# Kernel optimization log

Measured on AMD Instinct MI355X. Metric: run time of the kernel, lower is better.

The kernel has to match this reference:

```python
import jax, jax.numpy as jnp
import numpy as np

EMB = 128
HID = 256
VOCAB = 32000
B, LS, LT = 16, 256, 128


def _lstm(x_seq, h0, c0, Wk, Wr, b):
    """Keras-style LSTM (gate order i,f,g,o). x_seq: [B,T,D] -> ([B,T,H], h, c)."""
    xz = jnp.einsum('btd,dg->btg', x_seq, Wk) + b  # precompute input projection

    def step(carry, zt):
        h, c = carry
        z = zt + h @ Wr  # [B,4H]
        i, f, g, o = jnp.split(z, 4, axis=-1)
        c = jax.nn.sigmoid(f) * c + jax.nn.sigmoid(i) * jnp.tanh(g)
        h = jax.nn.sigmoid(o) * jnp.tanh(c)
        return (h, c), h

    (h, c), hs = jax.lax.scan(step, (h0, c0), xz.transpose(1, 0, 2))
    return hs.transpose(1, 0, 2), h, c


def setup_inputs() -> dict:
    key = jax.random.key(0)
    ks = jax.random.split(key, 12)
    sd_e = 1.0 / np.sqrt(EMB)
    sd_h = 1.0 / np.sqrt(HID)
    return {
        'x': jax.random.randint(ks[0], (B, LS), 0, VOCAB, dtype=jnp.int32),
        'y': jax.random.randint(ks[1], (B, LT), 0, VOCAB, dtype=jnp.int32),
        'enc_emb': jax.random.normal(ks[2], (VOCAB, EMB), jnp.float32) * 0.05,
        'enc_Wk': jax.random.normal(ks[3], (EMB, 4 * HID), jnp.float32) * sd_e,
        'enc_Wr': jax.random.normal(ks[4], (HID, 4 * HID), jnp.float32) * sd_h,
        'enc_b': jnp.zeros((4 * HID,), jnp.float32),
        'dec_emb': jax.random.normal(ks[5], (VOCAB, EMB), jnp.float32) * 0.05,
        'dec_Wk': jax.random.normal(ks[6], (EMB, 4 * HID), jnp.float32) * sd_e,
        'dec_Wr': jax.random.normal(ks[7], (HID, 4 * HID), jnp.float32) * sd_h,
        'dec_b': jnp.zeros((4 * HID,), jnp.float32),
        'Wout': jax.random.normal(ks[8], (2 * HID, VOCAB), jnp.float32) * (1.0 / np.sqrt(2 * HID)),
        'bout': jnp.zeros((VOCAB,), jnp.float32),
    }


def reference(x, y, enc_emb, enc_Wk, enc_Wr, enc_b, dec_emb, dec_Wk, dec_Wr, dec_b, Wout, bout):
    # ---- Encoder ----
    xe = enc_emb[x]  # [B,LS,EMB]
    z0 = jnp.zeros((x.shape[0], HID), jnp.float32)
    H, h, c = _lstm(xe, z0, z0, enc_Wk, enc_Wr, enc_b)  # H: [B,LS,HID]
    # ---- Decoder (teacher forcing) ----
    ye = dec_emb[y]  # [B,LT,EMB]
    S, hT, cT = _lstm(ye, h, c, dec_Wk, dec_Wr, dec_b)  # [B,LT,HID]
    S_ = jnp.concatenate([h[:, None, :], S[:, :-1, :]], axis=1)  # shifted states
    # Keras Attention (dot, no scale): A = softmax(S_ H^T) H
    scores = jnp.einsum('btd,bsd->bts', S_, H)  # [B,LT,LS]
    A = jnp.einsum('bts,bsd->btd', jax.nn.softmax(scores, axis=-1), H)
    feat = jnp.concatenate([S, A], axis=-1)  # [B,LT,2*HID]
    probs = jax.nn.softmax(feat @ Wout + bout, axis=-1)  # [B,LT,VOCAB]
    return probs
```

## Files before the change

### kernel.cpp

```cpp
#include <hip/hip_runtime.h>
#include <hip/hip_bf16.h>
#include <math.h>

#define BB    16
#define LS    256
#define LT    128
#define EMB   128
#define HID   256
#define G4    1024
#define VOCAB 32000

#define NSL   8
#define XROWS 112

typedef __attribute__((ext_vector_type(8))) short bf16x8;
typedef __attribute__((ext_vector_type(4))) float f32x4;
typedef __attribute__((ext_vector_type(4))) int   i32x4;
typedef unsigned short ushort_t;
typedef unsigned int uint_t;

__device__ inline float sigf(float x)      { return 1.0f / (1.0f + __expf(-x)); }
__device__ inline float tanhfast(float x)  { return 1.0f - 2.0f / (1.0f + __expf(2.0f * x)); }
__device__ inline ushort_t bf16_rne(float f) {
  __hip_bfloat16 h = __float2bfloat16(f);
  return *(ushort_t*)&h;
}

__global__ __launch_bounds__(256) void embed_proj_kernel(
    const int* __restrict__ x, const int* __restrict__ y,
    const float* __restrict__ eemb, const float* __restrict__ eWk,
    const float* __restrict__ eb,
    const float* __restrict__ demb, const float* __restrict__ dWk,
    const float* __restrict__ db,
    float* __restrict__ xze, float* __restrict__ xzd)
{
  const bool enc = blockIdx.x < 128;
  const int* idx = enc ? x : y;
  const float* emb = enc ? eemb : demb;
  const float* Wk  = enc ? eWk  : dWk;
  const float* bias= enc ? eb   : db;
  float* xz        = enc ? xze  : xzd;
  const int row0 = (enc ? blockIdx.x : blockIdx.x - 128) * 32;

  __shared__ float e[32][EMB];
  const int tid = threadIdx.x;

  for (int i = tid; i < 32 * EMB; i += 256) {
    int r = i >> 7, k = i & 127;
    int token = idx[row0 + r];
    e[r][k] = emb[(size_t)token * EMB + k];
  }
  __syncthreads();

  float acc[4][32];
#pragma unroll
  for (int q = 0; q < 4; ++q)
#pragma unroll
    for (int r = 0; r < 32; ++r) acc[q][r] = 0.0f;

  for (int k = 0; k < EMB; ++k) {
    float w0 = Wk[(size_t)k * G4 + 0 * 256 + tid];
    float w1 = Wk[(size_t)k * G4 + 1 * 256 + tid];
    float w2 = Wk[(size_t)k * G4 + 2 * 256 + tid];
    float w3 = Wk[(size_t)k * G4 + 3 * 256 + tid];
#pragma unroll
    for (int r = 0; r < 32; ++r) {
      float ev = e[r][k];
      acc[0][r] = fmaf(ev, w0, acc[0][r]);
      acc[1][r] = fmaf(ev, w1, acc[1][r]);
      acc[2][r] = fmaf(ev, w2, acc[2][r]);
      acc[3][r] = fmaf(ev, w3, acc[3][r]);
    }
  }
#pragma unroll
  for (int q = 0; q < 4; ++q) {
    float bb = bias[q * 256 + tid];
#pragma unroll
    for (int r = 0; r < 32; ++r)
      xz[(size_t)(row0 + r) * G4 + q * 256 + tid] = acc[q][r] + bb;
  }
}

__global__ __launch_bounds__(512, 1) void lstm_kernel(
    const float* __restrict__ xz,
    const float* __restrict__ Wr,
    const float* __restrict__ h0,
    int h0_stride,
    const float* __restrict__ cinit,
    float* __restrict__ Hout,
    float* __restrict__ c_fin,
    i32x4* __restrict__ fmb,
    int kid,
    int T)
{
  const int b    = blockIdx.x & (BB - 1);
  const int s    = blockIdx.x >> 4;
  const int tid  = threadIdx.x;
  const int lane = tid & 63;
  const int quarter = tid >> 7;
  const int col  = tid & 127;
  const int gate = col >> 5, u = col & 31;

  __shared__ float part[2][4][128];
  __shared__ float xbuf[XROWS][128];

  float w_r[64];
  {
    const float* wp = Wr + (size_t)(quarter * 64) * G4 + gate * 256 + s * 32 + u;
#pragma unroll
    for (int j = 0; j < 64; ++j) w_r[j] = wp[(size_t)j * G4];
  }

  const int i0 = quarter * 64 + lane;
  float hv = 0.0f;
  if (h0) hv = h0[(size_t)b * h0_stride + i0];

  float cs0 = 0.0f, cs1 = 0.0f;
  if (tid < 16 && cinit) {
    cs0 = cinit[b * HID + s * 32 + 2 * tid];
    cs1 = cinit[b * HID + s * 32 + 2 * tid + 1];
  }

  const int c0i = i0 >> 1;
  const int sel = i0 & 1;

  int tp = XROWS;
  for (int t = 0; t < T; ++t, ++tp) {
    if (tp >= XROWS) {
      __syncthreads();
      tp = 0;
      for (int tt = quarter; tt < XROWS; tt += 4) {
        int ts = t + tt;
        if (ts < T)
          xbuf[tt][col] = xz[((size_t)b * T + ts) * G4 + gate * 256 + s * 32 + u];
      }
    }

    float a0 = 0.0f, a1 = 0.0f, a2 = 0.0f, a3 = 0.0f;
#pragma unroll
    for (int j = 0; j < 64; j += 4) {
      a0 = fmaf(__int_as_float(__builtin_amdgcn_readlane(__float_as_int(hv), j + 0)), w_r[j + 0], a0);
      a1 = fmaf(__int_as_float(__builtin_amdgcn_readlane(__float_as_int(hv), j + 1)), w_r[j + 1], a1);
      a2 = fmaf(__int_as_float(__builtin_amdgcn_readlane(__float_as_int(hv), j + 2)), w_r[j + 2], a2);
      a3 = fmaf(__int_as_float(__builtin_amdgcn_readlane(__float_as_int(hv), j + 3)), w_r[j + 3], a3);
    }
    part[t & 1][quarter][col] = (a0 + a1) + (a2 + a3);
    __syncthreads();

    const int stamp = (t + 1) | (kid << 20);
    const size_t slot = (size_t)(b * 2 + (t & 1)) * 128;

    if (tid < 16) {
      const int ua = 2 * tid, ub = ua + 1;
      const float (*pp)[128] = part[t & 1];
      float p0a = pp[0][ua] + pp[1][ua] + pp[2][ua] + pp[3][ua];
      float p0b = pp[0][ub] + pp[1][ub] + pp[2][ub] + pp[3][ub];
      float p1a = pp[0][32 + ua] + pp[1][32 + ua] + pp[2][32 + ua] + pp[3][32 + ua];
      float p1b = pp[0][32 + ub] + pp[1][32 + ub] + pp[2][32 + ub] + pp[3][32 + ub];
      float p2a = pp[0][64 + ua] + pp[1][64 + ua] + pp[2][64 + ua] + pp[3][64 + ua];
      float p2b = pp[0][64 + ub] + pp[1][64 + ub] + pp[2][64 + ub] + pp[3][64 + ub];
      float p3a = pp[0][96 + ua] + pp[1][96 + ua] + pp[2][96 + ua] + pp[3][96 + ua];
      float p3b = pp[0][96 + ub] + pp[1][96 + ub] + pp[2][96 + ub] + pp[3][96 + ub];
      float2 xg0 = *(const float2*)&xbuf[tp][ua];
      float2 xg1 = *(const float2*)&xbuf[tp][32 + ua];
      float2 xg2 = *(const float2*)&xbuf[tp][64 + ua];
      float2 xg3 = *(const float2*)&xbuf[tp][96 + ua];

      float zi0 = p0a + xg0.x, zi1 = p0b + xg0.y;
      float zf0 = p1a + xg1.x, zf1 = p1b + xg1.y;
      float zg0 = p2a + xg2.x, zg1 = p2b + xg2.y;
      float zo0 = p3a + xg3.x, zo1 = p3b + xg3.y;

      cs0 = fmaf(sigf(zf0), cs0, sigf(zi0) * tanhfast(zg0));
      cs1 = fmaf(sigf(zf1), cs1, sigf(zi1) * tanhfast(zg1));
      float ha = sigf(zo0) * tanhfast(cs0);
      float hb = sigf(zo1) * tanhfast(cs1);

      *(float2*)&Hout[((size_t)b * T + t) * HID + s * 32 + ua] = make_float2(ha, hb);

      i32x4 ch;
      ch.x = __float_as_int(ha);
      ch.y = __float_as_int(hb);
      ch.z = ch.x ^ ch.y ^ stamp;
      ch.w = 0;
      const i32x4* fd = fmb + slot + s * 16 + tid;
      asm volatile("global_store_dwordx4 %0, %1, off sc0 sc1"
                   :: "v"(fd), "v"(ch) : "memory");
    }
    __syncthreads();

    if (t + 1 < T) {
      const i32x4* fp = fmb + slot + c0i;
      i32x4 v;
      for (;;) {
        asm volatile("global_load_dwordx4 %0, %1, off sc0 sc1\n\t"
                     "s_waitcnt vmcnt(0)"
                     : "=&v"(v) : "v"(fp) : "memory");
        if (v.z == (v.x ^ v.y ^ stamp)) break;
      }
      hv = __int_as_float(sel ? v.y : v.x);
    }
  }
  if (c_fin && tid < 16)
    *(float2*)&c_fin[b * HID + s * 32 + 2 * tid] = make_float2(cs0, cs1);
}

__global__ __launch_bounds__(256) void mid_kernel(
    const float* __restrict__ W, ushort_t* __restrict__ WT,
    const float* __restrict__ Henc, const float* __restrict__ S,
    __hip_bfloat16* __restrict__ featB)
{
  const int tid = threadIdx.x;

  if (blockIdx.x < 4000) {
    __shared__ float tile[64][65];
    const int nt = blockIdx.x % 500;
    const int kt = blockIdx.x / 500;
    const int n0 = nt * 64, k0 = kt * 64;
    const int r = tid >> 6, c = tid & 63;

#pragma unroll
    for (int q = 0; q < 16; ++q) {
      int kk = q * 4 + r;
      tile[kk][c] = W[(size_t)(k0 + kk) * VOCAB + n0 + c];
    }
    __syncthreads();

    const int nl = tid >> 2;
    const int seg = (tid & 3) * 16;
    uint_t o[8];
#pragma unroll
    for (int j = 0; j < 8; ++j) {
      uint_t lo = bf16_rne(tile[seg + 2 * j][nl]);
      uint_t hi = bf16_rne(tile[seg + 2 * j + 1][nl]);
      o[j] = lo | (hi << 16);
    }
    ushort_t* dst = WT + (size_t)(n0 + nl) * 512 + k0 + seg;
    ((uint4*)dst)[0] = make_uint4(o[0], o[1], o[2], o[3]);
    ((uint4*)dst)[1] = make_uint4(o[4], o[5], o[6], o[7]);
  } else {
    __shared__ float srow[HID];
    __shared__ float p[LS];
    __shared__ float sm[LS];

    const int m = blockIdx.x - 4000;
    const int b = m >> 7, t = m & (LT - 1);

    const float* s_ = (t == 0) ? (Henc + ((size_t)b * LS + (LS - 1)) * HID)
                               : (S + (size_t)(m - 1) * HID);
    srow[tid] = s_[tid];
    __syncthreads();

    const float4* h4 = (const float4*)(Henc + ((size_t)b * LS + tid) * HID);
    const float4* s4 = (const float4*)srow;
    float sc = 0.0f;
#pragma unroll 8
    for (int k = 0; k < HID / 4; ++k) {
      float4 a = h4[k], q = s4[k];
      sc += a.x * q.x + a.y * q.y + a.z * q.z + a.w * q.w;
    }
    sm[tid] = sc;
    __syncthreads();
    for (int st = 128; st > 0; st >>= 1) {
      if (tid < st) sm[tid] = fmaxf(sm[tid], sm[tid + st]);
      __syncthreads();
    }
    float mx = sm[0];
    __syncthreads();
    float e = __expf(sc - mx);
    p[tid] = e;
    sm[tid] = e;
    __syncthreads();
    for (int st = 128; st > 0; st >>= 1) {
      if (tid < st) sm[tid] += sm[tid + st];
      __syncthreads();
    }
    float inv = 1.0f / sm[0];

    float a_d = 0.0f;
#pragma unroll 4
    for (int s2 = 0; s2 < LS; ++s2)
      a_d = fmaf(p[s2], Henc[((size_t)b * LS + s2) * HID + tid], a_d);
    a_d *= inv;

    featB[(size_t)m * (2 * HID) + tid]       = __float2bfloat16(S[(size_t)m * HID + tid]);
    featB[(size_t)m * (2 * HID) + HID + tid] = __float2bfloat16(a_d);
  }
}

__global__ __launch_bounds__(256) void proj_exp_kernel(
    const ushort_t* __restrict__ A, const ushort_t* __restrict__ BT,
    const float* __restrict__ bout, float* __restrict__ rowsum,
    float* __restrict__ out)
{
  __shared__ ushort_t Ab[2][128 * 64];
  __shared__ ushort_t Bb[2][128 * 64];

  const int bid = blockIdx.x;
  const int k2 = (bid & 7) * 500 + (bid >> 3);
  const int mt = k2 & 15, nt = k2 >> 4;
  const int m0 = mt * 128, n0 = nt * 128;
  const int tid = threadIdx.x;
  const int wave = tid >> 6, lane = tid & 63;
  const int wm = wave >> 1, wn = wave & 1;
  const int r = lane & 15, kg = lane >> 4;

  const ushort_t* Ag = A + (size_t)m0 * 512;
  const ushort_t* Bg = BT + (size_t)n0 * 512;

  f32x4 acc[4][4];
#pragma unroll
  for (int i = 0; i < 4; ++i)
#pragma unroll
    for (int j = 0; j < 4; ++j) acc[i][j] = (f32x4){0.f, 0.f, 0.f, 0.f};

#define STAGE(kc, buf)                                                       \
  {                                                                          \
    _Pragma("unroll")                                                        \
    for (int q = 0; q < 4; ++q) {                                            \
      int L = q * 256 + tid;                                                 \
      int row_ = L >> 3, seg_ = L & 7;                                       \
      int so_ = row_ * 64 + ((seg_ ^ (row_ & 7)) << 3);                      \
      uint4 va_ = *(const uint4*)(Ag + (size_t)row_ * 512 + (kc) * 64 + seg_ * 8); \
      uint4 vb_ = *(const uint4*)(Bg + (size_t)row_ * 512 + (kc) * 64 + seg_ * 8); \
      *(uint4*)&Ab[buf][so_] = va_;                                          \
      *(uint4*)&Bb[buf][so_] = vb_;                                          \
    }                                                                        \
  }

  STAGE(0, 0);
  __syncthreads();

  for (int kc = 0; kc < 8; ++kc) {
    const int cur = kc & 1;
    if (kc < 7) STAGE(kc + 1, cur ^ 1);
#pragma unroll
    for (int ks = 0; ks < 2; ++ks) {
      bf16x8 a[4], b[4];
      const int seg = ks * 4 + kg;
#pragma unroll
      for (int i = 0; i < 4; ++i) {
        int row = wm * 64 + i * 16 + r;
        a[i] = *(const bf16x8*)&Ab[cur][row * 64 + ((seg ^ (row & 7)) << 3)];
      }
#pragma unroll
      for (int j = 0; j < 4; ++j) {
        int row = wn * 64 + j * 16 + r;
        b[j] = *(const bf16x8*)&Bb[cur][row * 64 + ((seg ^ (row & 7)) << 3)];
      }
#pragma unroll
      for (int i = 0; i < 4; ++i)
#pragma unroll
        for (int j = 0; j < 4; ++j)
          acc[i][j] = __builtin_amdgcn_mfma_f32_16x16x32_bf16(a[i], b[j], acc[i][j], 0, 0, 0);
    }
    __syncthreads();
  }
#undef STAGE

  float bv[4];
#pragma unroll
  for (int j = 0; j < 4; ++j) bv[j] = bout[n0 + wn * 64 + j * 16 + r];

#pragma unroll
  for (int i = 0; i < 4; ++i)
#pragma unroll
    for (int q = 0; q < 4; ++q) {
      const int row = m0 + wm * 64 + i * 16 + kg * 4 + q;
      float v = 0.0f;
#pragma unroll
      for (int j = 0; j < 4; ++j) {
        float e = __expf(acc[i][j][q] + bv[j]);
        out[(size_t)row * VOCAB + n0 + wn * 64 + j * 16 + r] = e;
        v += e;
      }
#pragma unroll
      for (int msk = 1; msk < 16; msk <<= 1) v += __shfl_xor(v, msk, 64);
      if (r == 0) atomicAdd(&rowsum[row], v);
    }
}

__global__ __launch_bounds__(256) void scale_kernel(
    float* __restrict__ out, const float* __restrict__ rowsum)
{
  const int row = blockIdx.x >> 2;
  const int seg = blockIdx.x & 3;
  const float s = 1.0f / rowsum[row];
  float4* o4 = (float4*)(out + (size_t)row * VOCAB) + seg * 2000;
  for (int i = threadIdx.x; i < 2000; i += 256) {
    float4 v = o4[i];
    v.x *= s; v.y *= s; v.z *= s; v.w *= s;
    o4[i] = v;
  }
}

extern "C" void kernel_launch(void* const* d_in, const int* in_sizes, int n_in,
                              void* d_out, int out_size, void* d_ws, size_t ws_size,
                              hipStream_t stream) {
  (void)in_sizes; (void)n_in; (void)out_size; (void)ws_size;

  const int*   x       = (const int*)d_in[0];
  const int*   y       = (const int*)d_in[1];
  const float* enc_emb = (const float*)d_in[2];
  const float* enc_Wk  = (const float*)d_in[3];
  const float* enc_Wr  = (const float*)d_in[4];
  const float* enc_b   = (const float*)d_in[5];
  const float* dec_emb = (const float*)d_in[6];
  const float* dec_Wk  = (const float*)d_in[7];
  const float* dec_Wr  = (const float*)d_in[8];
  const float* dec_b   = (const float*)d_in[9];
  const float* Wout    = (const float*)d_in[10];
  const float* bout    = (const float*)d_in[11];
  float* out = (float*)d_out;
  char*  ws  = (char*)d_ws;

  size_t off = 0;
  float* xz_enc = (float*)(ws + off); off += (size_t)BB * LS * G4 * 4;
  float* xz_dec = (float*)(ws + off); off += (size_t)BB * LT * G4 * 4;
  float* Henc   = (float*)(ws + off); off += (size_t)BB * LS * HID * 4;
  float* S      = (float*)(ws + off); off += (size_t)BB * LT * HID * 4;
  __hip_bfloat16* featB = (__hip_bfloat16*)(ws + off);
  off += (size_t)BB * LT * 2 * HID * 2;
  ushort_t* WoutT = (ushort_t*)(ws + off); off += (size_t)VOCAB * 512 * 2;
  float* c_fin  = (float*)(ws + off); off += (size_t)BB * HID * 4;
  size_t zero_base = off;
  float* rowsum = (float*)(ws + off); off += (size_t)BB * LT * 4;
  i32x4* fmb    = (i32x4*)(ws + off); off += (size_t)BB * 2 * 128 * 16;
  size_t zero_len = off - zero_base;

  hipMemsetAsync(ws + zero_base, 0, zero_len, stream);

  embed_proj_kernel<<<192, 256, 0, stream>>>(
      x, y, enc_emb, enc_Wk, enc_b, dec_emb, dec_Wk, dec_b, xz_enc, xz_dec);

  lstm_kernel<<<NSL * BB, 512, 0, stream>>>(
      xz_enc, enc_Wr, nullptr, 0, nullptr, Henc, c_fin, fmb, 0, LS);

  lstm_kernel<<<NSL * BB, 512, 0, stream>>>(
      xz_dec, dec_Wr, Henc + (size_t)(LS - 1) * HID, LS * HID, c_fin,
      S, nullptr, fmb, 1, LT);

  mid_kernel<<<4000 + BB * LT, 256, 0, stream>>>(
      Wout, WoutT, Henc, S, (__hip_bfloat16*)featB);

  proj_exp_kernel<<<16 * 250, 256, 0, stream>>>(
      (const ushort_t*)featB, WoutT, bout, rowsum, out);
  scale_kernel<<<4 * BB * LT, 256, 0, stream>>>(out, rowsum);
}
```

Measured before the change: 1.099 ms.

## Overlap encoder LSTM with Wout prepack and decoder embedding in one launch

Splits the embedding projection so the encoder input projection runs first. A combined launch then runs the latency-bound encoder LSTM blocks alongside the Wout transpose/bf16 prepack and the decoder input projection, so those independent jobs fill otherwise idle CUs. The attention part of the old mid kernel becomes its own kernel. The LSTM flag poll now keeps two loads in flight to cut spin latency. The risk is that the 128 LSTM blocks, which talk to each other through the flag mailbox, may not all be resident at once if filler blocks take the CUs first, which could slow progress or deadlock. The extra blocks also compete for memory bandwidth.

```diff
diff --git a/kernel.cpp b/kernel.cpp
--- a/kernel.cpp
+++ b/kernel.cpp
@@ -12,6 +12,7 @@
 
 #define NSL   8
 #define XROWS 112
+#define LSTM_POOL (4096 + XROWS * 128 * 4)
 
 typedef __attribute__((ext_vector_type(8))) short bf16x8;
 typedef __attribute__((ext_vector_type(4))) float f32x4;
@@ -26,24 +27,13 @@
   return *(ushort_t*)&h;
 }
 
-__global__ __launch_bounds__(256) void embed_proj_kernel(
-    const int* __restrict__ x, const int* __restrict__ y,
-    const float* __restrict__ eemb, const float* __restrict__ eWk,
-    const float* __restrict__ eb,
-    const float* __restrict__ demb, const float* __restrict__ dWk,
-    const float* __restrict__ db,
-    float* __restrict__ xze, float* __restrict__ xzd)
-{
-  const bool enc = blockIdx.x < 128;
-  const int* idx = enc ? x : y;
-  const float* emb = enc ? eemb : demb;
-  const float* Wk  = enc ? eWk  : dWk;
-  const float* bias= enc ? eb   : db;
-  float* xz        = enc ? xze  : xzd;
-  const int row0 = (enc ? blockIdx.x : blockIdx.x - 128) * 32;
-
-  __shared__ float e[32][EMB];
-  const int tid = threadIdx.x;
+__device__ __forceinline__ void embed_body(
+    char* pool, int row0, int tid,
+    const int* __restrict__ idx, const float* __restrict__ emb,
+    const float* __restrict__ Wk, const float* __restrict__ bias,
+    float* __restrict__ xz)
+{
+  float (*e)[EMB] = (float (*)[EMB])pool;
 
   for (int i = tid; i < 32 * EMB; i += 256) {
     int r = i >> 7, k = i & 127;
@@ -81,28 +71,55 @@
   }
 }
 
-__global__ __launch_bounds__(512, 1) void lstm_kernel(
-    const float* __restrict__ xz,
-    const float* __restrict__ Wr,
-    const float* __restrict__ h0,
-    int h0_stride,
+__device__ __forceinline__ void prepack_body(
+    char* pool, int tileIdx, int tid,
+    const float* __restrict__ W, ushort_t* __restrict__ WT)
+{
+  float (*tile)[65] = (float (*)[65])pool;
+  const int nt = tileIdx % 500;
+  const int kt = tileIdx / 500;
+  const int n0 = nt * 64, k0 = kt * 64;
+  const int r = tid >> 6, c = tid & 63;
+
+#pragma unroll
+  for (int q = 0; q < 16; ++q) {
+    int kk = q * 4 + r;
+    tile[kk][c] = W[(size_t)(k0 + kk) * VOCAB + n0 + c];
+  }
+  __syncthreads();
+
+  const int nl = tid >> 2;
+  const int seg = (tid & 3) * 16;
+  uint_t o[8];
+#pragma unroll
+  for (int j = 0; j < 8; ++j) {
+    uint_t lo = bf16_rne(tile[seg + 2 * j][nl]);
+    uint_t hi = bf16_rne(tile[seg + 2 * j + 1][nl]);
+    o[j] = lo | (hi << 16);
+  }
+  ushort_t* dst = WT + (size_t)(n0 + nl) * 512 + k0 + seg;
+  ((uint4*)dst)[0] = make_uint4(o[0], o[1], o[2], o[3]);
+  ((uint4*)dst)[1] = make_uint4(o[4], o[5], o[6], o[7]);
+}
+
+__device__ __forceinline__ void lstm_body(
+    char* pool, int bid,
+    const float* __restrict__ xz, const float* __restrict__ Wr,
+    const float* __restrict__ h0, int h0_stride,
     const float* __restrict__ cinit,
-    float* __restrict__ Hout,
-    float* __restrict__ c_fin,
-    i32x4* __restrict__ fmb,
-    int kid,
-    int T)
-{
-  const int b    = blockIdx.x & (BB - 1);
-  const int s    = blockIdx.x >> 4;
+    float* __restrict__ Hout, float* __restrict__ c_fin,
+    i32x4* __restrict__ fmb, int kid, int T)
+{
+  float (*part)[4][128] = (float (*)[4][128])pool;
+  float (*xbuf)[128]    = (float (*)[128])(pool + 4096);
+
+  const int b    = bid & (BB - 1);
+  const int s    = bid >> 4;
   const int tid  = threadIdx.x;
   const int lane = tid & 63;
   const int quarter = tid >> 7;
   const int col  = tid & 127;
   const int gate = col >> 5, u = col & 31;
-
-  __shared__ float part[2][4][128];
-  __shared__ float xbuf[XROWS][128];
 
   float w_r[64];
   {
@@ -191,13 +208,22 @@
 
     if (t + 1 < T) {
       const i32x4* fp = fmb + slot + c0i;
-      i32x4 v;
+      i32x4 va, vb, v;
+      asm volatile("global_load_dwordx4 %0, %1, off sc0 sc1"
+                   : "=v"(va) : "v"(fp) : "memory");
+      asm volatile("global_load_dwordx4 %0, %1, off sc0 sc1"
+                   : "=v"(vb) : "v"(fp) : "memory");
       for (;;) {
-        asm volatile("global_load_dwordx4 %0, %1, off sc0 sc1\n\t"
-                     "s_waitcnt vmcnt(0)"
-                     : "=&v"(v) : "v"(fp) : "memory");
-        if (v.z == (v.x ^ v.y ^ stamp)) break;
+        asm volatile("s_waitcnt vmcnt(1)" : "+v"(va) :: "memory");
+        if (va.z == (va.x ^ va.y ^ stamp)) { v = va; break; }
+        asm volatile("global_load_dwordx4 %0, %1, off sc0 sc1"
+                     : "=v"(va) : "v"(fp) : "memory");
+        asm volatile("s_waitcnt vmcnt(1)" : "+v"(vb) :: "memory");
+        if (vb.z == (vb.x ^ vb.y ^ stamp)) { v = vb; break; }
+        asm volatile("global_load_dwordx4 %0, %1, off sc0 sc1"
+                     : "=v"(vb) : "v"(fp) : "memory");
       }
+      asm volatile("s_waitcnt vmcnt(0)" : "+v"(va), "+v"(vb) :: "memory");
       hv = __int_as_float(sel ? v.y : v.x);
     }
   }
@@ -205,87 +231,102 @@
     *(float2*)&c_fin[b * HID + s * 32 + 2 * tid] = make_float2(cs0, cs1);
 }
 
-__global__ __launch_bounds__(256) void mid_kernel(
-    const float* __restrict__ W, ushort_t* __restrict__ WT,
+__global__ __launch_bounds__(256) void embed_enc_kernel(
+    const int* __restrict__ x, const float* __restrict__ emb,
+    const float* __restrict__ Wk, const float* __restrict__ bias,
+    float* __restrict__ xz)
+{
+  __shared__ float poolf[32 * EMB];
+  embed_body((char*)poolf, blockIdx.x * 32, threadIdx.x, x, emb, Wk, bias, xz);
+}
+
+__global__ __launch_bounds__(512, 1) void enc_stage_kernel(
+    const float* __restrict__ xz_enc, const float* __restrict__ enc_Wr,
+    float* __restrict__ Henc, float* __restrict__ c_fin,
+    i32x4* __restrict__ fmb,
+    const float* __restrict__ Wout, ushort_t* __restrict__ WoutT,
+    const int* __restrict__ y, const float* __restrict__ dec_emb,
+    const float* __restrict__ dec_Wk, const float* __restrict__ dec_b,
+    float* __restrict__ xz_dec)
+{
+  extern __shared__ char pool[];
+  const int bid = blockIdx.x;
+  if (bid < 128) {
+    lstm_body(pool, bid, xz_enc, enc_Wr, nullptr, 0, nullptr,
+              Henc, c_fin, fmb, 0, LS);
+  } else if (bid < 2128) {
+    const int half = threadIdx.x >> 8, t256 = threadIdx.x & 255;
+    prepack_body(pool + half * 16640, 2 * (bid - 128) + half, t256, Wout, WoutT);
+  } else {
+    const int half = threadIdx.x >> 8, t256 = threadIdx.x & 255;
+    embed_body(pool + half * 16384, ((bid - 2128) * 2 + half) * 32, t256,
+               y, dec_emb, dec_Wk, dec_b, xz_dec);
+  }
+}
+
+__global__ __launch_bounds__(512, 1) void lstm_kernel(
+    const float* __restrict__ xz, const float* __restrict__ Wr,
+    const float* __restrict__ h0, int h0_stride,
+    const float* __restrict__ cinit,
+    float* __restrict__ Hout, float* __restrict__ c_fin,
+    i32x4* __restrict__ fmb, int kid, int T)
+{
+  extern __shared__ char pool[];
+  lstm_body(pool, blockIdx.x, xz, Wr, h0, h0_stride, cinit,
+            Hout, c_fin, fmb, kid, T);
+}
+
+__global__ __launch_bounds__(256) void attn_kernel(
     const float* __restrict__ Henc, const float* __restrict__ S,
     __hip_bfloat16* __restrict__ featB)
 {
+  const int m = blockIdx.x;
+  const int b = m >> 7, t = m & (LT - 1);
   const int tid = threadIdx.x;
 
-  if (blockIdx.x < 4000) {
-    __shared__ float tile[64][65];
-    const int nt = blockIdx.x % 500;
-    const int kt = blockIdx.x / 500;
-    const int n0 = nt * 64, k0 = kt * 64;
-    const int r = tid >> 6, c = tid & 63;
-
-#pragma unroll
-    for (int q = 0; q < 16; ++q) {
-      int kk = q * 4 + r;
-      tile[kk][c] = W[(size_t)(k0 + kk) * VOCAB + n0 + c];
-    }
+  __shared__ float srow[HID];
+  __shared__ float p[LS];
+  __shared__ float sm[LS];
+
+  const float* s_ = (t == 0) ? (Henc + ((size_t)b * LS + (LS - 1)) * HID)
+                             : (S + (size_t)(m - 1) * HID);
+  srow[tid] = s_[tid];
+  __syncthreads();
+
+  const float4* h4 = (const float4*)(Henc + ((size_t)b * LS + tid) * HID);
+  const float4* s4 = (const float4*)srow;
+  float sc = 0.0f;
+#pragma unroll 8
+  for (int k = 0; k < HID / 4; ++k) {
+    float4 a = h4[k], q = s4[k];
+    sc += a.x * q.x + a.y * q.y + a.z * q.z + a.w * q.w;
+  }
+  sm[tid] = sc;
+  __syncthreads();
+  for (int st = 128; st > 0; st >>= 1) {
+    if (tid < st) sm[tid] = fmaxf(sm[tid], sm[tid + st]);
     __syncthreads();
-
-    const int nl = tid >> 2;
-    const int seg = (tid & 3) * 16;
-    uint_t o[8];
-#pragma unroll
-    for (int j = 0; j < 8; ++j) {
-      uint_t lo = bf16_rne(tile[seg + 2 * j][nl]);
-      uint_t hi = bf16_rne(tile[seg + 2 * j + 1][nl]);
-      o[j] = lo | (hi << 16);
-    }
-    ushort_t* dst = WT + (size_t)(n0 + nl) * 512 + k0 + seg;
-    ((uint4*)dst)[0] = make_uint4(o[0], o[1], o[2], o[3]);
-    ((uint4*)dst)[1] = make_uint4(o[4], o[5], o[6], o[7]);
-  } else {
-    __shared__ float srow[HID];
-    __shared__ float p[LS];
-    __shared__ float sm[LS];
-
-    const int m = blockIdx.x - 4000;
-    const int b = m >> 7, t = m & (LT - 1);
-
-    const float* s_ = (t == 0) ? (Henc + ((size_t)b * LS + (LS - 1)) * HID)
-                               : (S + (size_t)(m - 1) * HID);
-    srow[tid] = s_[tid];
+  }
+  float mx = sm[0];
+  __syncthreads();
+  float e = __expf(sc - mx);
+  p[tid] = e;
+  sm[tid] = e;
+  __syncthreads();
+  for (int st = 128; st > 0; st >>= 1) {
+    if (tid < st) sm[tid] += sm[tid + st];
     __syncthreads();
-
-    const float4* h4 = (const float4*)(Henc + ((size_t)b * LS + tid) * HID);
-    const float4* s4 = (const float4*)srow;
-    float sc = 0.0f;
-#pragma unroll 8
-    for (int k = 0; k < HID / 4; ++k) {
-      float4 a = h4[k], q = s4[k];
-      sc += a.x * q.x + a.y * q.y + a.z * q.z + a.w * q.w;
-    }
-    sm[tid] = sc;
-    __syncthreads();
-    for (int st = 128; st > 0; st >>= 1) {
-      if (tid < st) sm[tid] = fmaxf(sm[tid], sm[tid + st]);
-      __syncthreads();
-    }
-    float mx = sm[0];
-    __syncthreads();
-    float e = __expf(sc - mx);
-    p[tid] = e;
-    sm[tid] = e;
-    __syncthreads();
-    for (int st = 128; st > 0; st >>= 1) {
-      if (tid < st) sm[tid] += sm[tid + st];
-      __syncthreads();
-    }
-    float inv = 1.0f / sm[0];
-
-    float a_d = 0.0f;
+  }
+  float inv = 1.0f / sm[0];
+
+  float a_d = 0.0f;
 #pragma unroll 4
-    for (int s2 = 0; s2 < LS; ++s2)
-      a_d = fmaf(p[s2], Henc[((size_t)b * LS + s2) * HID + tid], a_d);
-    a_d *= inv;
-
-    featB[(size_t)m * (2 * HID) + tid]       = __float2bfloat16(S[(size_t)m * HID + tid]);
-    featB[(size_t)m * (2 * HID) + HID + tid] = __float2bfloat16(a_d);
-  }
+  for (int s2 = 0; s2 < LS; ++s2)
+    a_d = fmaf(p[s2], Henc[((size_t)b * LS + s2) * HID + tid], a_d);
+  a_d *= inv;
+
+  featB[(size_t)m * (2 * HID) + tid]       = __float2bfloat16(S[(size_t)m * HID + tid]);
+  featB[(size_t)m * (2 * HID) + HID + tid] = __float2bfloat16(a_d);
 }
 
 __global__ __launch_bounds__(256) void proj_exp_kernel(
@@ -430,18 +471,17 @@
 
   hipMemsetAsync(ws + zero_base, 0, zero_len, stream);
 
-  embed_proj_kernel<<<192, 256, 0, stream>>>(
-      x, y, enc_emb, enc_Wk, enc_b, dec_emb, dec_Wk, dec_b, xz_enc, xz_dec);
-
-  lstm_kernel<<<NSL * BB, 512, 0, stream>>>(
-      xz_enc, enc_Wr, nullptr, 0, nullptr, Henc, c_fin, fmb, 0, LS);
-
-  lstm_kernel<<<NSL * BB, 512, 0, stream>>>(
+  embed_enc_kernel<<<128, 256, 0, stream>>>(x, enc_emb, enc_Wk, enc_b, xz_enc);
+
+  enc_stage_kernel<<<2160, 512, LSTM_POOL, stream>>>(
+      xz_enc, enc_Wr, Henc, c_fin, fmb,
+      Wout, WoutT, y, dec_emb, dec_Wk, dec_b, xz_dec);
+
+  lstm_kernel<<<NSL * BB, 512, LSTM_POOL, stream>>>(
       xz_dec, dec_Wr, Henc + (size_t)(LS - 1) * HID, LS * HID, c_fin,
       S, nullptr, fmb, 1, LT);
 
-  mid_kernel<<<4000 + BB * LT, 256, 0, stream>>>(
-      Wout, WoutT, Henc, S, (__hip_bfloat16*)featB);
+  attn_kernel<<<BB * LT, 256, 0, stream>>>(Henc, S, featB);
 
   proj_exp_kernel<<<16 * 250, 256, 0, stream>>>(
       (const ushort_t*)featB, WoutT, bout, rowsum, out);
```

After: 1.144 ms. +4.1%, slower.

## Pipeline LSTM flag polling and use direct global-to-LDS loads in projection GEMM

Applied to the files above, without the earlier changes.

The LSTM cross-block handoff now keeps two flag loads in flight and waits on vmcnt(1) between them, so a new poll is always outstanding instead of one full round trip per check. The LSTM shared arrays move into a dynamically sized pool behind a device-function body, which looks like groundwork for fusing kernels. The projection GEMM staging replaces register-mediated global→LDS copies with global_load_lds, applying the XOR swizzle on the global source address. The intent is lower handoff latency in the serial recurrence and less VGPR and instruction traffic when staging the GEMM. The risk is that the GEMM has no explicit vmcnt wait before its barrier, and that the LDS layout must exactly match what the fragment reads expect.

```diff
diff --git a/kernel.cpp b/kernel.cpp
--- a/kernel.cpp
+++ b/kernel.cpp
@@ -12,6 +12,7 @@
 
 #define NSL   8
 #define XROWS 112
+#define LSTM_POOL (4096 + XROWS * 128 * 4)
 
 typedef __attribute__((ext_vector_type(8))) short bf16x8;
 typedef __attribute__((ext_vector_type(4))) float f32x4;
@@ -81,28 +82,24 @@
   }
 }
 
-__global__ __launch_bounds__(512, 1) void lstm_kernel(
-    const float* __restrict__ xz,
-    const float* __restrict__ Wr,
-    const float* __restrict__ h0,
-    int h0_stride,
+__device__ __forceinline__ void lstm_body(
+    char* pool, int bid,
+    const float* __restrict__ xz, const float* __restrict__ Wr,
+    const float* __restrict__ h0, int h0_stride,
     const float* __restrict__ cinit,
-    float* __restrict__ Hout,
-    float* __restrict__ c_fin,
-    i32x4* __restrict__ fmb,
-    int kid,
-    int T)
-{
-  const int b    = blockIdx.x & (BB - 1);
-  const int s    = blockIdx.x >> 4;
+    float* __restrict__ Hout, float* __restrict__ c_fin,
+    i32x4* __restrict__ fmb, int kid, int T)
+{
+  float (*part)[4][128] = (float (*)[4][128])pool;
+  float (*xbuf)[128]    = (float (*)[128])(pool + 4096);
+
+  const int b    = bid & (BB - 1);
+  const int s    = bid >> 4;
   const int tid  = threadIdx.x;
   const int lane = tid & 63;
   const int quarter = tid >> 7;
   const int col  = tid & 127;
   const int gate = col >> 5, u = col & 31;
-
-  __shared__ float part[2][4][128];
-  __shared__ float xbuf[XROWS][128];
 
   float w_r[64];
   {
@@ -191,18 +188,39 @@
 
     if (t + 1 < T) {
       const i32x4* fp = fmb + slot + c0i;
-      i32x4 v;
+      i32x4 va, vb, v;
+      asm volatile("global_load_dwordx4 %0, %1, off sc0 sc1"
+                   : "=v"(va) : "v"(fp) : "memory");
+      asm volatile("global_load_dwordx4 %0, %1, off sc0 sc1"
+                   : "=v"(vb) : "v"(fp) : "memory");
       for (;;) {
-        asm volatile("global_load_dwordx4 %0, %1, off sc0 sc1\n\t"
-                     "s_waitcnt vmcnt(0)"
-                     : "=&v"(v) : "v"(fp) : "memory");
-        if (v.z == (v.x ^ v.y ^ stamp)) break;
+        asm volatile("s_waitcnt vmcnt(1)" : "+v"(va) :: "memory");
+        if (va.z == (va.x ^ va.y ^ stamp)) { v = va; break; }
+        asm volatile("global_load_dwordx4 %0, %1, off sc0 sc1"
+                     : "=v"(va) : "v"(fp) : "memory");
+        asm volatile("s_waitcnt vmcnt(1)" : "+v"(vb) :: "memory");
+        if (vb.z == (vb.x ^ vb.y ^ stamp)) { v = vb; break; }
+        asm volatile("global_load_dwordx4 %0, %1, off sc0 sc1"
+                     : "=v"(vb) : "v"(fp) : "memory");
       }
+      asm volatile("s_waitcnt vmcnt(0)" : "+v"(va), "+v"(vb) :: "memory");
       hv = __int_as_float(sel ? v.y : v.x);
     }
   }
   if (c_fin && tid < 16)
     *(float2*)&c_fin[b * HID + s * 32 + 2 * tid] = make_float2(cs0, cs1);
+}
+
+__global__ __launch_bounds__(512, 1) void lstm_kernel(
+    const float* __restrict__ xz, const float* __restrict__ Wr,
+    const float* __restrict__ h0, int h0_stride,
+    const float* __restrict__ cinit,
+    float* __restrict__ Hout, float* __restrict__ c_fin,
+    i32x4* __restrict__ fmb, int kid, int T)
+{
+  extern __shared__ char pool[];
+  lstm_body(pool, blockIdx.x, xz, Wr, h0, h0_stride, cinit,
+            Hout, c_fin, fmb, kid, T);
 }
 
 __global__ __launch_bounds__(256) void mid_kernel(
@@ -314,18 +332,25 @@
 #pragma unroll
     for (int j = 0; j < 4; ++j) acc[i][j] = (f32x4){0.f, 0.f, 0.f, 0.f};
 
-#define STAGE(kc, buf)                                                       \
-  {                                                                          \
-    _Pragma("unroll")                                                        \
-    for (int q = 0; q < 4; ++q) {                                            \
-      int L = q * 256 + tid;                                                 \
-      int row_ = L >> 3, seg_ = L & 7;                                       \
-      int so_ = row_ * 64 + ((seg_ ^ (row_ & 7)) << 3);                      \
-      uint4 va_ = *(const uint4*)(Ag + (size_t)row_ * 512 + (kc) * 64 + seg_ * 8); \
-      uint4 vb_ = *(const uint4*)(Bg + (size_t)row_ * 512 + (kc) * 64 + seg_ * 8); \
-      *(uint4*)&Ab[buf][so_] = va_;                                          \
-      *(uint4*)&Bb[buf][so_] = vb_;                                          \
-    }                                                                        \
+#define STAGE(kc, buf)                                                        \
+  {                                                                           \
+    _Pragma("unroll")                                                         \
+    for (int q = 0; q < 4; ++q) {                                             \
+      int L = q * 256 + tid;                                                  \
+      int row_ = L >> 3, seg_ = L & 7;                                        \
+      int sseg_ = seg_ ^ (row_ & 7);                                          \
+      int wbase = (q * 256 + (tid & ~63)) * 8;   \
+      __builtin_amdgcn_global_load_lds(                                       \
+          (const __attribute__((address_space(1))) unsigned int*)             \
+              (Ag + (size_t)row_ * 512 + (kc) * 64 + sseg_ * 8),              \
+          (__attribute__((address_space(3))) unsigned int*)&Ab[buf][wbase],   \
+          16, 0, 0);                                                          \
+      __builtin_amdgcn_global_load_lds(                                       \
+          (const __attribute__((address_space(1))) unsigned int*)             \
+              (Bg + (size_t)row_ * 512 + (kc) * 64 + sseg_ * 8),              \
+          (__attribute__((address_space(3))) unsigned int*)&Bb[buf][wbase],   \
+          16, 0, 0);                                                          \
+    }                                                                         \
   }
 
   STAGE(0, 0);
@@ -433,10 +458,10 @@
   embed_proj_kernel<<<192, 256, 0, stream>>>(
       x, y, enc_emb, enc_Wk, enc_b, dec_emb, dec_Wk, dec_b, xz_enc, xz_dec);
 
-  lstm_kernel<<<NSL * BB, 512, 0, stream>>>(
+  lstm_kernel<<<NSL * BB, 512, LSTM_POOL, stream>>>(
       xz_enc, enc_Wr, nullptr, 0, nullptr, Henc, c_fin, fmb, 0, LS);
 
-  lstm_kernel<<<NSL * BB, 512, 0, stream>>>(
+  lstm_kernel<<<NSL * BB, 512, LSTM_POOL, stream>>>(
       xz_dec, dec_Wr, Henc + (size_t)(LS - 1) * HID, LS * HID, c_fin,
       S, nullptr, fmb, 1, LT);
 
```

Measured after the change: 1.152 ms. 4.8% more time.
